# Kernel tuning notes

Measured on AMD Instinct MI355X. Metric: run time of the kernel, lower is better.

Reference implementation:

```python
import jax, jax.numpy as jnp
import numpy as np

N = 10000      # nodes
E = 160000     # edges
MUL = 64       # multiplicity of 0e and 1o in node feats / target
NATTR = 10     # number of element types (node_attrs one-hot width)
RDIM = 8       # radial (edge_feats) dim
NAVG = 16.0    # num_avg_neighbors
_INV3 = 0.5773502691896258  # CG coeff for 1o x 1o -> 0e (1/sqrt(3))


def setup_inputs() -> dict:
    key = jax.random.key(0)
    ks = jax.random.split(key, 20)
    return {
        "node_attrs": jax.random.uniform(ks[0], (N, NATTR), jnp.float32),
        "node_feats": jax.random.normal(ks[1], (N, 4 * MUL), jnp.float32),
        "edge_attrs_real": jax.random.normal(ks[2], (E, 4), jnp.float32),
        "edge_attrs_imag": jax.random.normal(ks[3], (E, 4), jnp.float32),
        "edge_feats": jax.random.normal(ks[4], (E, RDIM), jnp.float32),
        # linear_up (per-l internal weights)
        "W_up0": jax.random.normal(ks[5], (MUL, MUL), jnp.float32),
        "W_up1": jax.random.normal(ks[6], (MUL, MUL), jnp.float32),
        # conv_tp_weights MLP: [8, 64, 64, 64, 4*MUL]
        "M1": jax.random.normal(ks[7], (RDIM, 64), jnp.float32),
        "M2": jax.random.normal(ks[8], (64, 64), jnp.float32),
        "M3": jax.random.normal(ks[9], (64, 64), jnp.float32),
        "M4": jax.random.normal(ks[10], (64, 4 * MUL), jnp.float32),
        # linear: irreps_mid (128x0e+128x1o) -> irreps_nonlin (128x0e+64x1o)
        "W_lin_s": jax.random.normal(ks[11], (2 * MUL, 2 * MUL), jnp.float32),
        "W_lin_v": jax.random.normal(ks[12], (2 * MUL, MUL), jnp.float32),
        # skip_tp: FullyConnectedTensorProduct(node_feats, node_attrs -> irreps_nonlin)
        "W_sk_s": jax.random.normal(ks[13], (MUL, NATTR, 2 * MUL), jnp.float32),
        "W_sk_v": jax.random.normal(ks[14], (MUL, NATTR, MUL), jnp.float32),
        "edge_index": jax.random.randint(ks[15], (2, E), 0, N, jnp.int64
                                         if jax.config.jax_enable_x64 else jnp.int32),
    }


def _forward(node_attrs, node_feats, edge_attrs_real, edge_attrs_imag, edge_feats,
             W_up0, W_up1, M1, M2, M3, M4, W_lin_s, W_lin_v, W_sk_s, W_sk_v,
             sender, receiver):
    n = node_feats.shape[0]
    x0 = node_feats[:, :MUL]                          # (N, 64)   64x0e
    x1 = node_feats[:, MUL:].reshape(n, MUL, 3)       # (N, 64, 3) 64x1o

    # skip TP (fully connected, node_attrs are scalars)
    sk_norm = 1.0 / np.sqrt(MUL * NATTR)
    sc_s = jnp.einsum('nu,na,uav->nv', x0, node_attrs, W_sk_s) * sk_norm   # (N,128)
    sc_v = jnp.einsum('nui,na,uav->nvi', x1, node_attrs, W_sk_v) * sk_norm # (N,64,3)

    # linear_up (per-l)
    up_norm = 1.0 / np.sqrt(MUL)
    x0 = (x0 @ W_up0) * up_norm
    x1 = jnp.einsum('nui,uv->nvi', x1, W_up1) * up_norm

    # radial MLP -> per-edge TP weights (4 uvu paths x MUL)
    h = jax.nn.silu((edge_feats @ M1) / np.sqrt(RDIM))
    h = jax.nn.silu((h @ M2) / 8.0)
    h = jax.nn.silu((h @ M3) / 8.0)
    tw = (h @ M4) / 8.0                               # (E, 256)
    wA, wB, wC, wD = (tw[:, :MUL], tw[:, MUL:2*MUL],
                      tw[:, 2*MUL:3*MUL], tw[:, 3*MUL:])

    xs0 = x0[sender]                                  # (E, 64)
    xs1 = x1[sender]                                  # (E, 64, 3)

    def conv_tp(y):
        # y: (E,4) = [0e | 1o]; uvu paths with per-edge weights
        y0, y1 = y[:, :1], y[:, 1:]
        s = jnp.concatenate([xs0 * y0 * wA,                                  # 0e x 0e -> 0e
                             jnp.einsum('eui,ei->eu', xs1, y1) * _INV3 * wD  # 1o x 1o -> 0e
                             ], axis=1)                                      # (E,128)
        v = jnp.concatenate([(xs0 * wB)[:, :, None] * y1[:, None, :],        # 0e x 1o -> 1o
                             xs1 * (y0 * wC)[:, :, None]                     # 1o x 0e -> 1o
                             ], axis=1)                                      # (E,128,3)
        return s, v

    sr, vr = conv_tp(edge_attrs_real)
    si, vi = conv_tp(edge_attrs_imag)

    ms_r = jax.ops.segment_sum(sr, receiver, num_segments=n)
    mv_r = jax.ops.segment_sum(vr, receiver, num_segments=n)
    ms_i = jax.ops.segment_sum(si, receiver, num_segments=n)
    mv_i = jax.ops.segment_sum(vi, receiver, num_segments=n)

    lin_norm = (1.0 / np.sqrt(2 * MUL)) / (2.0 * NAVG)

    def lin(ms, mv):
        return (ms @ W_lin_s) * lin_norm, jnp.einsum('nui,uv->nvi', mv, W_lin_v) * lin_norm

    def gate(s, v):
        # irreps_nonlin = 64x0e scalars | 64x0e gates | 64x1o gated
        scal = jax.nn.silu(s[:, :MUL])
        g = jax.nn.silu(s[:, MUL:])
        return jnp.concatenate([scal, (v * g[:, :, None]).reshape(n, 3 * MUL)], axis=1)

    ls, lv = lin(ms_r, mv_r)
    real = gate(ls + sc_s, lv + sc_v)                 # (N, 256), residual on real part
    lsi, lvi = lin(ms_i, mv_i)
    imag = gate(lsi, lvi)                             # (N, 256)

    # view_as_complex + reshape [N, num_features, dim//num_features]; complex kept
    # as trailing real/imag axis of size 2.
    return jnp.stack([real, imag], axis=-1).reshape(n, MUL, (4 * MUL) // MUL, 2)


def reference(node_attrs, node_feats, edge_attrs_real, edge_attrs_imag, edge_feats,
              W_up0, W_up1, M1, M2, M3, M4, W_lin_s, W_lin_v, W_sk_s, W_sk_v,
              edge_index):
    sender, receiver = edge_index[0], edge_index[1]
    return _forward(node_attrs, node_feats, edge_attrs_real, edge_attrs_imag,
                    edge_feats, W_up0, W_up1, M1, M2, M3, M4,
                    W_lin_s, W_lin_v, W_sk_s, W_sk_v, sender, receiver)
```

## Files before the change

kernel.cpp:

```cpp
#include <hip/hip_runtime.h>
#include <hip/hip_bf16.h>

#define NN 10000
#define NE 160000
#define NGRP 625
#define XPLN 640000

#define SK_NORM   0.039528470752104741f
#define UP_NORM   0.125f
#define M1_NORM   0.35355339059327373f
#define INV3      0.5773502691896258f
#define LIN_NORM  0.0027621358640099516f

__device__ __forceinline__ float siluf(float x) { return x / (1.0f + __expf(-x)); }

__device__ __forceinline__ unsigned short f2bf_bits(float x) {
    union { __hip_bfloat16 h; unsigned short u; } cv;
    cv.h = __float2bfloat16(x);
    return cv.u;
}
__device__ __forceinline__ float bflo(unsigned int w) { return __uint_as_float(w << 16); }
__device__ __forceinline__ float bfhi(unsigned int w) { return __uint_as_float(w & 0xffff0000u); }

typedef short bf16x8 __attribute__((ext_vector_type(8)));
typedef float f32x4  __attribute__((ext_vector_type(4)));

__global__ __launch_bounds__(256) void k_detect(const int* __restrict__ ei32, int* __restrict__ flag) {
    __shared__ int cnt;
    if (threadIdx.x == 0) cnt = 0;
    __syncthreads();
    int z = 0;
    for (int i = threadIdx.x; i < 1024; i += 256)
        if (ei32[2 * i + 1] == 0) z++;
    atomicAdd(&cnt, z);
    __syncthreads();
    if (threadIdx.x == 0) flag[0] = (cnt >= 512) ? 1 : 0;
}

__global__ __launch_bounds__(256) void k_cvt(const int* __restrict__ ei32, const int* __restrict__ flag,
                                             int* __restrict__ snd, int* __restrict__ rcv) {
    int e = blockIdx.x * 256 + threadIdx.x;
    if (e >= NE) return;
    if (flag[0]) {
        const long long* e64 = (const long long*)ei32;
        snd[e] = (int)e64[e];
        rcv[e] = (int)e64[NE + e];
    } else {
        snd[e] = ei32[e];
        rcv[e] = ei32[NE + e];
    }
}

__global__ __launch_bounds__(256) void k_wprepN(
    const float* __restrict__ Wsk_s, const float* __restrict__ Wsk_v,
    const float* __restrict__ Wu0, const float* __restrict__ Wu1,
    unsigned short* __restrict__ WNF) {
    int idx = blockIdx.x * 256 + threadIdx.x;
    if (idx >= 131072) return;
    float val;
    if (idx < 81920) {
        int p = idx / 10240, r = idx % 10240;
        int kc = r >> 9, l8 = r & 511;
        int lane = l8 >> 3, j = l8 & 7, quad = lane >> 4, lo = lane & 15;
        int a = kc >> 1, u = (kc & 1) * 32 + quad * 8 + j;
        val = Wsk_s[(u * 10 + a) * 128 + p * 16 + lo];
    } else if (idx < 122880) {
        int rel = idx - 81920;
        int p = rel / 10240, r = rel % 10240;
        int kc = r >> 9, l8 = r & 511;
        int lane = l8 >> 3, j = l8 & 7, quad = lane >> 4, lo = lane & 15;
        int a = kc >> 1, u = (kc & 1) * 32 + quad * 8 + j;
        val = Wsk_v[(u * 10 + a) * 64 + p * 16 + lo];
    } else if (idx < 126976) {
        int rel = idx - 122880;
        int p = rel >> 10, r = rel & 1023;
        int kc = r >> 9, l8 = r & 511;
        int lane = l8 >> 3, j = l8 & 7, quad = lane >> 4, lo = lane & 15;
        int u = kc * 32 + quad * 8 + j;
        val = Wu0[u * 64 + p * 16 + lo];
    } else {
        int rel = idx - 126976;
        int p = rel >> 10, r = rel & 1023;
        int kc = r >> 9, l8 = r & 511;
        int lane = l8 >> 3, j = l8 & 7, quad = lane >> 4, lo = lane & 15;
        int u = kc * 32 + quad * 8 + j;
        val = Wu1[u * 64 + p * 16 + lo];
    }
    WNF[idx] = f2bf_bits(val);
}

__global__ __launch_bounds__(256) void k_xprep(
    const float* __restrict__ node_attrs, const float* __restrict__ node_feats,
    unsigned short* __restrict__ xpk, float* __restrict__ attrsP) {
    int idx = blockIdx.x * 256 + threadIdx.x;
    if (idx < 4 * NN * 64) {
        int n = idx >> 8, c = idx & 255;
        int plane = c >> 6, u = c & 63;
        float v = (plane == 0) ? node_feats[(long)n * 256 + u]
                               : node_feats[(long)n * 256 + 64 + u * 3 + (plane - 1)];
        xpk[(size_t)plane * XPLN + (long)n * 64 + u] = f2bf_bits(v);
        return;
    }
    int i2 = idx - 4 * NN * 64;
    if (i2 < 10 * NN) {
        int a = i2 / NN, n = i2 - a * NN;
        attrsP[i2] = node_attrs[(long)n * 10 + a];
    }
}

__global__ __launch_bounds__(256) void k_wprep2(
    const float* __restrict__ M1, const float* __restrict__ M2,
    const float* __restrict__ M3, const float* __restrict__ M4,
    const float* __restrict__ W_lin_s, const float* __restrict__ W_lin_v,
    unsigned short* __restrict__ WFG, unsigned short* __restrict__ WLF) {
    int idx = blockIdx.x * 256 + threadIdx.x;
    if (idx >= (52 + 48) * 512) return;
    if (idx < 52 * 512) {
        int f = idx >> 9, r = idx & 511;
        int lane = r >> 3, j = r & 7;
        int quad = lane >> 4, lo = lane & 15;
        float val;
        if (f < 4) {
            int n = f * 16 + lo, k = quad * 8 + j;
            val = (k < 8) ? M1[k * 64 + n] : 0.f;
        } else if (f < 12) {
            int g2 = f - 4, nt = g2 >> 1, half = g2 & 1;
            int n = nt * 16 + lo, k = half * 32 + quad * 8 + j;
            val = M2[k * 64 + n];
        } else if (f < 20) {
            int g3 = f - 12, nt = g3 >> 1, half = g3 & 1;
            int n = nt * 16 + lo, k = half * 32 + quad * 8 + j;
            val = M3[k * 64 + n];
        } else {
            int g4 = f - 20, tt = g4 >> 1, half = g4 & 1;
            int n = tt * 16 + lo, k = half * 32 + quad * 8 + j;
            val = M4[k * 256 + n];
        }
        WFG[idx] = f2bf_bits(val);
    } else {
        int rel = idx - 52 * 512;
        int f = rel >> 9, r = rel & 511;
        int lane = r >> 3, j = r & 7;
        int quad = lane >> 4, lo = lane & 15;
        float val;
        if (f < 32) {
            int vt = f >> 2, ks = f & 3;
            val = W_lin_s[(ks * 32 + quad * 8 + j) * 128 + vt * 16 + lo];
        } else {
            int f2 = f - 32;
            int vt = f2 >> 2, ks = f2 & 3;
            val = W_lin_v[(ks * 32 + quad * 8 + j) * 64 + vt * 16 + lo];
        }
        WLF[rel] = f2bf_bits(val);
    }
}

#define G0 8
#define NB0 79
#define G2 4
#define NB2 157
#define G3 16
#define NB3 40
#define KNODE_GRID (4*NB0 + 2*NB2 + 2*NB3)

__global__ __launch_bounds__(128) void k_node(
    const unsigned short* __restrict__ xpk, const float* __restrict__ attrsP,
    const unsigned short* __restrict__ WNF,
    float* __restrict__ sc_s, float* __restrict__ sc_v,
    float* __restrict__ x0u, float* __restrict__ x1p) {
    __shared__ unsigned short pan[2 * 10240];
    __shared__ float att[10 * 128];

    int t = threadIdx.x;
    int bid = blockIdx.x;
    int type, vp, chunk;
    if (bid < 4 * NB0)                 { type = 0; vp = bid / NB0; chunk = bid % NB0; }
    else if (bid < 4 * NB0 + 2 * NB2)  { int r = bid - 4 * NB0; type = 2; vp = r / NB2; chunk = r % NB2; }
    else                               { int r = bid - 4 * NB0 - 2 * NB2; type = 3; vp = r / NB3; chunk = r % NB3; }
    int G = (type == 0) ? G0 : (type == 2 ? G2 : G3);
    int g0 = chunk * G;
    int ng = NGRP - g0; if (ng > G) ng = G;
    int n0 = g0 * 16;

    int psrc, pcnt;
    if (type == 0)      { psrc = vp * 2 * 10240;           pcnt = 20480; }
    else if (type == 2) { psrc = 81920 + vp * 2 * 10240;   pcnt = 20480; }
    else                { psrc = 122880 + vp * 2 * 1024;   pcnt = 2048;  }
    for (int i = t; i < pcnt / 8; i += 128)
        ((float4*)pan)[i] = ((const float4*)(WNF + psrc))[i];
    if (type == 3) {
        for (int i = t; i < 2048 / 8; i += 128)
            ((float4*)(pan + 2048))[i] = ((const float4*)(WNF + 126976 + vp * 2 * 1024))[i];
    }
    if (type <= 2) {
        int cnt = ng * 16;
        #pragma unroll
        for (int k = 0; k < 10; k++) {
            int i = k * 128 + t;
            int nl = t;
            if (nl < cnt) att[i] = attrsP[k * NN + n0 + nl];
        }
    }
    __syncthreads();

    int wv = t >> 6, lane = t & 63, lo = lane & 15, quad = lane >> 4;
    int lbase = lane * 8;
    const f32x4 zacc = {0.f, 0.f, 0.f, 0.f};
    const unsigned short* mypan = pan + wv * 10240;

    if (type == 0) {
        int vtg = vp * 2 + wv;
        const unsigned short* xb = xpk;
        bf16x8 nfa0 = *(const bf16x8*)(xb + (long)(n0 + lo) * 64 + quad * 8);
        bf16x8 nfa1 = *(const bf16x8*)(xb + (long)(n0 + lo) * 64 + 32 + quad * 8);
        #pragma unroll 1
        for (int g = 0; g < ng; g++) {
            bf16x8 fa0 = nfa0, fa1 = nfa1;
            if (g + 1 < ng) {
                nfa0 = *(const bf16x8*)(xb + (long)(n0 + (g + 1) * 16 + lo) * 64 + quad * 8);
                nfa1 = *(const bf16x8*)(xb + (long)(n0 + (g + 1) * 16 + lo) * 64 + 32 + quad * 8);
            }
            f32x4 acc = zacc;
            #pragma unroll
            for (int a = 0; a < 10; a++) {
                bf16x8 b0 = *(const bf16x8*)&mypan[(2 * a) * 512 + lbase];
                bf16x8 b1 = *(const bf16x8*)&mypan[(2 * a + 1) * 512 + lbase];
                f32x4 p = __builtin_amdgcn_mfma_f32_16x16x32_bf16(fa0, b0, zacc, 0, 0, 0);
                p = __builtin_amdgcn_mfma_f32_16x16x32_bf16(fa1, b1, p, 0, 0, 0);
                float4 afv = *(const float4*)&att[a * 128 + g * 16 + quad * 4];
                acc[0] += afv.x * p[0]; acc[1] += afv.y * p[1];
                acc[2] += afv.z * p[2]; acc[3] += afv.w * p[3];
            }
            int nb = n0 + g * 16;
            #pragma unroll
            for (int r = 0; r < 4; r++)
                sc_s[(long)(nb + quad * 4 + r) * 128 + vtg * 16 + lo] = acc[r] * SK_NORM;
        }
    } else if (type == 2) {
        int vt = vp * 2 + wv;
        bf16x8 nfa0[3], nfa1[3];
        #pragma unroll
        for (int i = 0; i < 3; i++) {
            const unsigned short* xb = xpk + (size_t)(1 + i) * XPLN + (long)(n0 + lo) * 64;
            nfa0[i] = *(const bf16x8*)(xb + quad * 8);
            nfa1[i] = *(const bf16x8*)(xb + 32 + quad * 8);
        }
        #pragma unroll 1
        for (int g = 0; g < ng; g++) {
            bf16x8 fa0[3], fa1[3];
            #pragma unroll
            for (int i = 0; i < 3; i++) { fa0[i] = nfa0[i]; fa1[i] = nfa1[i]; }
            if (g + 1 < ng) {
                #pragma unroll
                for (int i = 0; i < 3; i++) {
                    const unsigned short* xb = xpk + (size_t)(1 + i) * XPLN + (long)(n0 + (g + 1) * 16 + lo) * 64;
                    nfa0[i] = *(const bf16x8*)(xb + quad * 8);
                    nfa1[i] = *(const bf16x8*)(xb + 32 + quad * 8);
                }
            }
            f32x4 acc0 = zacc, acc1 = zacc, acc2 = zacc;
            #pragma unroll
            for (int a = 0; a < 10; a++) {
                bf16x8 b0 = *(const bf16x8*)&mypan[(2 * a) * 512 + lbase];
                bf16x8 b1 = *(const bf16x8*)&mypan[(2 * a + 1) * 512 + lbase];
                float4 afv = *(const float4*)&att[a * 128 + g * 16 + quad * 4];
                f32x4 p0 = __builtin_amdgcn_mfma_f32_16x16x32_bf16(fa0[0], b0, zacc, 0, 0, 0);
                p0 = __builtin_amdgcn_mfma_f32_16x16x32_bf16(fa1[0], b1, p0, 0, 0, 0);
                acc0[0] += afv.x * p0[0]; acc0[1] += afv.y * p0[1];
                acc0[2] += afv.z * p0[2]; acc0[3] += afv.w * p0[3];
                f32x4 p1 = __builtin_amdgcn_mfma_f32_16x16x32_bf16(fa0[1], b0, zacc, 0, 0, 0);
                p1 = __builtin_amdgcn_mfma_f32_16x16x32_bf16(fa1[1], b1, p1, 0, 0, 0);
                acc1[0] += afv.x * p1[0]; acc1[1] += afv.y * p1[1];
                acc1[2] += afv.z * p1[2]; acc1[3] += afv.w * p1[3];
                f32x4 p2 = __builtin_amdgcn_mfma_f32_16x16x32_bf16(fa0[2], b0, zacc, 0, 0, 0);
                p2 = __builtin_amdgcn_mfma_f32_16x16x32_bf16(fa1[2], b1, p2, 0, 0, 0);
                acc2[0] += afv.x * p2[0]; acc2[1] += afv.y * p2[1];
                acc2[2] += afv.z * p2[2]; acc2[3] += afv.w * p2[3];
            }
            int nb = n0 + g * 16;
            #pragma unroll
            for (int r = 0; r < 4; r++) {
                long rb = (long)(nb + quad * 4 + r) * 192 + vt * 16 + lo;
                sc_v[rb]       = acc0[r] * SK_NORM;
                sc_v[rb + 64]  = acc1[r] * SK_NORM;
                sc_v[rb + 128] = acc2[r] * SK_NORM;
            }
        }
    } else {
        int vt = vp * 2 + wv;
        bf16x8 bk20 = *(const bf16x8*)&pan[wv * 1024 + lbase];
        bf16x8 bk21 = *(const bf16x8*)&pan[wv * 1024 + 512 + lbase];
        bf16x8 bk30 = *(const bf16x8*)&pan[2048 + wv * 1024 + lbase];
        bf16x8 bk31 = *(const bf16x8*)&pan[2048 + wv * 1024 + 512 + lbase];
        #pragma unroll 1
        for (int g = 0; g < ng; g++) {
            int nb = n0 + g * 16;
            {
                const unsigned short* xb = xpk + (long)(nb + lo) * 64;
                bf16x8 fa0 = *(const bf16x8*)(xb + quad * 8);
                bf16x8 fa1 = *(const bf16x8*)(xb + 32 + quad * 8);
                f32x4 acc = __builtin_amdgcn_mfma_f32_16x16x32_bf16(fa0, bk20, zacc, 0, 0, 0);
                acc = __builtin_amdgcn_mfma_f32_16x16x32_bf16(fa1, bk21, acc, 0, 0, 0);
                #pragma unroll
                for (int r = 0; r < 4; r++)
                    x0u[(long)(nb + quad * 4 + r) * 64 + vt * 16 + lo] = acc[r] * UP_NORM;
            }
            #pragma unroll
            for (int i = 0; i < 3; i++) {
                const unsigned short* xb = xpk + (size_t)(1 + i) * XPLN + (long)(nb + lo) * 64;
                bf16x8 fa0 = *(const bf16x8*)(xb + quad * 8);
                bf16x8 fa1 = *(const bf16x8*)(xb + 32 + quad * 8);
                f32x4 acc = __builtin_amdgcn_mfma_f32_16x16x32_bf16(fa0, bk30, zacc, 0, 0, 0);
                acc = __builtin_amdgcn_mfma_f32_16x16x32_bf16(fa1, bk31, acc, 0, 0, 0);
                #pragma unroll
                for (int r = 0; r < 4; r++)
                    x1p[(size_t)i * XPLN + (long)(nb + quad * 4 + r) * 64 + vt * 16 + lo] = acc[r] * UP_NORM;
            }
        }
    }
}

__global__ __launch_bounds__(256) void k_hist(const int* __restrict__ rcv, int* __restrict__ counts) {
    int e = blockIdx.x * 256 + threadIdx.x;
    if (e < NE) atomicAdd(&counts[rcv[e]], 1);
}

__global__ __launch_bounds__(1024) void k_scan(const int* __restrict__ counts, int* __restrict__ offsets) {
    __shared__ int partial[1024];
    int t = threadIdx.x;
    const int CHUNK = (NN + 1023) / 1024;
    int base = t * CHUNK;
    int s = 0;
    for (int i = 0; i < CHUNK; i++) if (base + i < NN) s += counts[base + i];
    partial[t] = s;
    __syncthreads();
    for (int d = 1; d < 1024; d *= 2) {
        int v = (t >= d) ? partial[t - d] : 0;
        __syncthreads();
        partial[t] += v;
        __syncthreads();
    }
    int excl = (t == 0) ? 0 : partial[t - 1];
    for (int i = 0; i < CHUNK; i++) {
        if (base + i < NN) { offsets[base + i] = excl; excl += counts[base + i]; }
    }
    if (t == 1023) offsets[NN] = partial[1023];
}

__global__ __launch_bounds__(256) void k_fill(const int* __restrict__ rcv, const int* __restrict__ snd,
                                              const int* __restrict__ offsets,
                                              int* __restrict__ cursor, int2* __restrict__ epk) {
    int e = blockIdx.x * 256 + threadIdx.x;
    if (e < NE) {
        int r = rcv[e];
        int pos = atomicAdd(&cursor[r], 1);
        epk[offsets[r] + pos] = make_int2(snd[e], e);
    }
}

__global__ __launch_bounds__(256) void k_eprep(const int2* __restrict__ epk,
                                               const float4* __restrict__ ear, const float4* __restrict__ eai,
                                               const float4* __restrict__ ef,
                                               int* __restrict__ sndp,
                                               float4* __restrict__ earp, float4* __restrict__ eaip,
                                               float4* __restrict__ efp) {
    int j = blockIdx.x * 256 + threadIdx.x;
    if (j >= NE) return;
    int2 se = epk[j];
    sndp[j] = se.x;
    earp[j] = ear[se.y];
    eaip[j] = eai[se.y];
    efp[(long)j * 2]     = ef[(long)se.y * 2];
    efp[(long)j * 2 + 1] = ef[(long)se.y * 2 + 1];
}

#define HID_STRIDE 72
#define OB_STRIDE  40
#define EPB 256
#define EMW 8

__global__ __launch_bounds__(512) void k_edge_mlp(
    const float4* __restrict__ efp, const unsigned short* __restrict__ WFG,
    __hip_bfloat16* __restrict__ twp) {
    __shared__ unsigned short wfrag[52 * 512];
    __shared__ unsigned short hid[EMW][16 * HID_STRIDE];

    int t = threadIdx.x;
    for (int i = t; i < 52 * 512 / 8; i += 512)
        ((float4*)wfrag)[i] = ((const float4*)WFG)[i];
    __syncthreads();

    int wv = t >> 6;
    int lane = t & 63;
    int lo = lane & 15;
    int quad = lane >> 4;
    int lbase = lane * 8;
    unsigned short* myhid = hid[wv];
    unsigned short* myob  = hid[wv];
    const f32x4 zacc = {0.f, 0.f, 0.f, 0.f};

    float4 f0, f1;
    if (quad == 0) {
        long jb0 = (long)blockIdx.x * EPB + wv * 16;
        f0 = efp[(jb0 + lo) * 2];
        f1 = efp[(jb0 + lo) * 2 + 1];
    }

    #pragma unroll 1
    for (int g = 0; g < EPB / 128; g++) {
        long jbase = (long)blockIdx.x * EPB + g * 128 + wv * 16;

        bf16x8 a1 = {0, 0, 0, 0, 0, 0, 0, 0};
        if (quad == 0) {
            union { unsigned short us[8]; bf16x8 v; } pk;
            pk.us[0] = f2bf_bits(f0.x * M1_NORM); pk.us[1] = f2bf_bits(f0.y * M1_NORM);
            pk.us[2] = f2bf_bits(f0.z * M1_NORM); pk.us[3] = f2bf_bits(f0.w * M1_NORM);
            pk.us[4] = f2bf_bits(f1.x * M1_NORM); pk.us[5] = f2bf_bits(f1.y * M1_NORM);
            pk.us[6] = f2bf_bits(f1.z * M1_NORM); pk.us[7] = f2bf_bits(f1.w * M1_NORM);
            a1 = pk.v;
            if (g + 1 < EPB / 128) {
                long jbn = jbase + 128;
                f0 = efp[(jbn + lo) * 2];
                f1 = efp[(jbn + lo) * 2 + 1];
            }
        }
        {
            f32x4 acc[4];
            #pragma unroll
            for (int nt = 0; nt < 4; nt++) {
                bf16x8 b = *(const bf16x8*)&wfrag[nt * 512 + lbase];
                acc[nt] = __builtin_amdgcn_mfma_f32_16x16x32_bf16(a1, b, zacc, 0, 0, 0);
            }
            #pragma unroll
            for (int nt = 0; nt < 4; nt++)
                #pragma unroll
                for (int r = 0; r < 4; r++)
                    myhid[(quad * 4 + r) * HID_STRIDE + nt * 16 + lo] = f2bf_bits(siluf(acc[nt][r]));
        }

        #pragma unroll
        for (int L = 0; L < 2; L++) {
            int fb = 4 + L * 8;
            bf16x8 a0 = *(const bf16x8*)&myhid[lo * HID_STRIDE + quad * 8];
            bf16x8 a1v = *(const bf16x8*)&myhid[lo * HID_STRIDE + 32 + quad * 8];
            f32x4 acc[4];
            #pragma unroll
            for (int nt = 0; nt < 4; nt++) {
                bf16x8 b0 = *(const bf16x8*)&wfrag[(fb + nt * 2) * 512 + lbase];
                bf16x8 b1 = *(const bf16x8*)&wfrag[(fb + nt * 2 + 1) * 512 + lbase];
                acc[nt] = __builtin_amdgcn_mfma_f32_16x16x32_bf16(a0, b0, zacc, 0, 0, 0);
                acc[nt] = __builtin_amdgcn_mfma_f32_16x16x32_bf16(a1v, b1, acc[nt], 0, 0, 0);
            }
            #pragma unroll
            for (int nt = 0; nt < 4; nt++)
                #pragma unroll
                for (int r = 0; r < 4; r++)
                    myhid[(quad * 4 + r) * HID_STRIDE + nt * 16 + lo] = f2bf_bits(siluf(acc[nt][r] * 0.125f));
        }

        {
            bf16x8 a0 = *(const bf16x8*)&myhid[lo * HID_STRIDE + quad * 8];
            bf16x8 a1v = *(const bf16x8*)&myhid[lo * HID_STRIDE + 32 + quad * 8];
            int sedge = lane >> 2, sch = lane & 3;
            #pragma unroll 1
            for (int rd = 0; rd < 8; rd++) {
                f32x4 acc2[2];
                #pragma unroll
                for (int p = 0; p < 2; p++) {
                    int tt = (rd < 4) ? (p * 4 + rd) : (8 + p * 4 + (rd - 4));
                    bf16x8 b0 = *(const bf16x8*)&wfrag[(20 + tt * 2) * 512 + lbase];
                    bf16x8 b1 = *(const bf16x8*)&wfrag[(20 + tt * 2 + 1) * 512 + lbase];
                    acc2[p] = __builtin_amdgcn_mfma_f32_16x16x32_bf16(a0, b0, zacc, 0, 0, 0);
                    acc2[p] = __builtin_amdgcn_mfma_f32_16x16x32_bf16(a1v, b1, acc2[p], 0, 0, 0);
                }
                #pragma unroll
                for (int p = 0; p < 2; p++)
                    #pragma unroll
                    for (int r = 0; r < 4; r++)
                        myob[(quad * 4 + r) * OB_STRIDE + 2 * lo + p] = f2bf_bits(acc2[p][r] * 0.125f);
                bf16x8 vv = *(const bf16x8*)&myob[sedge * OB_STRIDE + sch * 8];
                *(bf16x8*)(twp + (jbase + sedge) * 256 + rd * 32 + sch * 8) = vv;
            }
        }
    }
}

#define NPB 4
#define CB2 4
__global__ __launch_bounds__(256) void k_conv(
    const int* __restrict__ offsets, const int* __restrict__ sndp,
    const float4* __restrict__ earp, const float4* __restrict__ eaip,
    const float* __restrict__ x0u, const float* __restrict__ x1p,
    const __hip_bfloat16* __restrict__ twp,
    unsigned short* __restrict__ msgF) {
    __shared__ unsigned short stg[NPB][1024];
    int t = threadIdx.x;
    int wv = t >> 6;
    int u = t & 63;
    int n = blockIdx.x * NPB + wv;
    int beg = offsets[n], end = offsets[n + 1];
    const int tsel0 = 2 * u, tsel1 = 128 + 2 * u;
    float a0r = 0.f, a1r = 0.f, a2r = 0.f, a3r = 0.f;
    float a0i = 0.f, a1i = 0.f, a2i = 0.f, a3i = 0.f;
    float c0r = 0.f, c1r = 0.f, c2r = 0.f, c3r = 0.f;
    float c0i = 0.f, c1i = 0.f, c2i = 0.f, c3i = 0.f;

    for (int jb = beg; jb < end; jb += CB2) {
        unsigned int t0[CB2], t1[CB2];
        float x0v[CB2], xv0[CB2], xv1[CB2], xv2[CB2];
        float4 yr[CB2], yi[CB2];
        #pragma unroll
        for (int p = 0; p < CB2; p++) {
            int j = jb + p;
            int jc = (j < end) ? j : (end - 1);
            int s = sndp[jc];
            yr[p] = earp[jc];
            yi[p] = eaip[jc];
            long sb = (long)s * 64 + u;
            x0v[p] = x0u[sb];
            xv0[p] = x1p[sb];
            xv1[p] = x1p[XPLN + sb];
            xv2[p] = x1p[2 * XPLN + sb];
            bool valid = (j < end);
            t0[p] = valid ? *(const unsigned int*)(twp + (long)jc * 256 + tsel0) : 0u;
            t1[p] = valid ? *(const unsigned int*)(twp + (long)jc * 256 + tsel1) : 0u;
        }
        #pragma unroll
        for (int p = 0; p < CB2; p++) {
            float wA = bflo(t0[p]), wB = bfhi(t0[p]);
            float xa = x0v[p] * wA, xb = x0v[p] * wB;
            a0r += xa * yr[p].x; a1r += xb * yr[p].y; a2r += xb * yr[p].z; a3r += xb * yr[p].w;
            a0i += xa * yi[p].x; a1i += xb * yi[p].y; a2i += xb * yi[p].z; a3i += xb * yi[p].w;
            float wC = bflo(t1[p]), wDs = bfhi(t1[p]) * INV3;
            float dr = xv0[p] * yr[p].y + xv1[p] * yr[p].z + xv2[p] * yr[p].w;
            float di = xv0[p] * yi[p].y + xv1[p] * yi[p].z + xv2[p] * yi[p].w;
            c0r += dr * wDs; c0i += di * wDs;
            float ycr = yr[p].x * wC, yci = yi[p].x * wC;
            c1r += xv0[p] * ycr; c2r += xv1[p] * ycr; c3r += xv2[p] * ycr;
            c1i += xv0[p] * yci; c2i += xv1[p] * yci; c3i += xv2[p] * yci;
        }
    }

    unsigned short* sg = stg[wv];
    sg[u]       = f2bf_bits(a0r);
    sg[128 + u] = f2bf_bits(a0i);
    sg[256 + u] = f2bf_bits(a1r);
    sg[384 + u] = f2bf_bits(a2r);
    sg[512 + u] = f2bf_bits(a3r);
    sg[640 + u] = f2bf_bits(a1i);
    sg[768 + u] = f2bf_bits(a2i);
    sg[896 + u] = f2bf_bits(a3i);
    sg[64 + u]  = f2bf_bits(c0r);
    sg[192 + u] = f2bf_bits(c0i);
    sg[320 + u] = f2bf_bits(c1r);
    sg[448 + u] = f2bf_bits(c2r);
    sg[576 + u] = f2bf_bits(c3r);
    sg[704 + u] = f2bf_bits(c1i);
    sg[832 + u] = f2bf_bits(c2i);
    sg[960 + u] = f2bf_bits(c3i);
    __syncthreads();

    #pragma unroll
    for (int rep = 0; rep < 2; rep++) {
        int job = rep * 256 + t;
        int m = job >> 7, c = job & 127;
        int nm = blockIdx.x * NPB + m;
        int g = nm >> 4, lo = nm & 15;
        bf16x8 vv = *(const bf16x8*)&stg[m][c * 8];
        *(bf16x8*)(msgF + (size_t)g * 16384 + (c >> 2) * 512 + lo * 32 + (c & 3) * 8) = vv;
    }
}

#define SV_STRIDE 129
#define VV_STRIDE 65

__global__ __launch_bounds__(256, 3) void k_lin(
    const unsigned short* __restrict__ msgF,
    const float* __restrict__ sc_s, const float* __restrict__ sc_v,
    const unsigned short* __restrict__ WLF,
    float* __restrict__ out) {
    __shared__ char smem[49152];
    unsigned short* wfrag = (unsigned short*)smem;
    float* sval = (float*)smem;
    float* vval = (float*)(smem + 2 * 16 * SV_STRIDE * 4);

    int t = threadIdx.x;
    for (int i = t; i < 48 * 512 / 8; i += 256)
        ((float4*)wfrag)[i] = ((const float4*)WLF)[i];
    __syncthreads();

    int wv = t >> 6;
    int lane = t & 63;
    int lo = lane & 15;
    int quad = lane >> 4;
    int lbase = lane * 8;
    int aoff_lane = lo * 32 + quad * 8;
    const f32x4 zacc = {0.f, 0.f, 0.f, 0.f};

    long g = blockIdx.x;
    long nbase = g * 16;
    const unsigned short* agbase = msgF + (size_t)g * 16384;

    f32x4 accs[10];
    #pragma unroll
    for (int q = 0; q < 10; q++) {
        int tau = wv + q * 4;
        int cblk, fb;
        if (tau < 16) {
            int ri = tau >> 3, vt = tau & 7;
            cblk = ri; fb = vt * 4;
        } else {
            int tp = tau - 16;
            int ri = tp / 12, rem = tp % 12;
            int i = rem >> 2, vt = rem & 3;
            cblk = 2 + ri * 3 + i; fb = 32 + vt * 4;
        }
        f32x4 acc = zacc;
        #pragma unroll
        for (int ks = 0; ks < 4; ks++) {
            bf16x8 a = *(const bf16x8*)(agbase + (cblk * 4 + ks) * 512 + aoff_lane);
            bf16x8 b = *(const bf16x8*)&wfrag[(fb + ks) * 512 + lbase];
            acc = __builtin_amdgcn_mfma_f32_16x16x32_bf16(a, b, acc, 0, 0, 0);
        }
        accs[q] = acc;
    }
    __syncthreads();

    #pragma unroll
    for (int q = 0; q < 10; q++) {
        int tau = wv + q * 4;
        if (tau < 16) {
            int ri = tau >> 3, vt = tau & 7;
            int cidx = (ri * 16) * SV_STRIDE + vt * 16 + lo;
            #pragma unroll
            for (int r = 0; r < 4; r++)
                sval[cidx + (quad * 4 + r) * SV_STRIDE] = accs[q][r] * LIN_NORM;
        } else {
            int tp = tau - 16;
            int ri = tp / 12, rem = tp % 12;
            int i = rem >> 2, vt = rem & 3;
            int cidx = ((ri * 3 + i) * 16) * VV_STRIDE + vt * 16 + lo;
            #pragma unroll
            for (int r = 0; r < 4; r++)
                vval[cidx + (quad * 4 + r) * VV_STRIDE] = accs[q][r] * LIN_NORM;
        }
    }
    __syncthreads();

    #pragma unroll 1
    for (int j = 0; j < 16; j++) {
        int c = t;
        long gn = nbase + j;
        float re, im;
        if (c < 64) {
            float sr = sval[(0 * 16 + j) * SV_STRIDE + c] + sc_s[gn * 128 + c];
            float si = sval[(1 * 16 + j) * SV_STRIDE + c];
            re = siluf(sr); im = siluf(si);
        } else {
            int rem = c - 64;
            int v = rem / 3;
            int i = rem - v * 3;
            float gr = siluf(sval[(0 * 16 + j) * SV_STRIDE + 64 + v] + sc_s[gn * 128 + 64 + v]);
            float gi = siluf(sval[(1 * 16 + j) * SV_STRIDE + 64 + v]);
            float lr = vval[((0 * 3 + i) * 16 + j) * VV_STRIDE + v] + sc_v[gn * 192 + i * 64 + v];
            float li = vval[((1 * 3 + i) * 16 + j) * VV_STRIDE + v];
            re = lr * gr; im = li * gi;
        }
        ((float2*)out)[gn * 256 + c] = make_float2(re, im);
    }
}

extern "C" void kernel_launch(void* const* d_in, const int* in_sizes, int n_in,
                              void* d_out, int out_size, void* d_ws, size_t ws_size,
                              hipStream_t stream) {
    const float* node_attrs = (const float*)d_in[0];
    const float* node_feats = (const float*)d_in[1];
    const float* ear        = (const float*)d_in[2];
    const float* eai        = (const float*)d_in[3];
    const float* edge_feats = (const float*)d_in[4];
    const float* W_up0      = (const float*)d_in[5];
    const float* W_up1      = (const float*)d_in[6];
    const float* M1         = (const float*)d_in[7];
    const float* M2         = (const float*)d_in[8];
    const float* M3         = (const float*)d_in[9];
    const float* M4         = (const float*)d_in[10];
    const float* W_lin_s    = (const float*)d_in[11];
    const float* W_lin_v    = (const float*)d_in[12];
    const float* W_sk_s     = (const float*)d_in[13];
    const float* W_sk_v     = (const float*)d_in[14];
    const int*   ei         = (const int*)d_in[15];

    char* ws = (char*)d_ws;
    size_t o_x0u = 0;
    size_t o_x1p = o_x0u + (size_t)NN * 64 * 4;
    size_t o_scs = o_x1p + (size_t)NN * 256 * 4;
    size_t o_scv = o_scs + (size_t)NN * 128 * 4;
    size_t o_tw  = o_scv + (size_t)NN * 192 * 4;
    size_t o_cnt = o_tw  + (size_t)NE * 256 * 2;
    size_t o_cur = o_cnt + (size_t)NN * 4;
    size_t o_ofs = o_cur + (size_t)NN * 4;
    size_t o_epk = o_ofs + (size_t)(NN + 1) * 4 + 60;
    size_t o_snd = o_epk + (size_t)NE * 8;
    size_t o_rcv = o_snd + (size_t)NE * 4;
    size_t o_flg = o_rcv + (size_t)NE * 4;
    size_t o_msg = o_flg + 64;
    size_t o_wnf = o_msg + (size_t)NN * 1024 * 2;
    size_t o_snp = o_wnf + 262144;
    size_t o_erp = o_snp + (size_t)NE * 4;
    size_t o_eip = o_erp + (size_t)NE * 16;
    size_t o_efp = o_eip + (size_t)NE * 16;
    size_t o_wfg = o_efp + (size_t)NE * 32;
    size_t o_wlf = o_wfg + (size_t)52 * 512 * 2;
    size_t o_xpk = o_wlf + (size_t)48 * 512 * 2;
    size_t o_atp = o_xpk + (size_t)4 * NN * 64 * 2;

    float* x0u = (float*)(ws + o_x0u);
    float* x1p = (float*)(ws + o_x1p);
    float* sc_s = (float*)(ws + o_scs);
    float* sc_v = (float*)(ws + o_scv);
    __hip_bfloat16* twp = (__hip_bfloat16*)(ws + o_tw);
    int* counts  = (int*)(ws + o_cnt);
    int* cursor  = (int*)(ws + o_cur);
    int* offsets = (int*)(ws + o_ofs);
    int2* epk    = (int2*)(ws + o_epk);
    int* snd     = (int*)(ws + o_snd);
    int* rcv     = (int*)(ws + o_rcv);
    int* flag    = (int*)(ws + o_flg);
    unsigned short* msgF = (unsigned short*)(ws + o_msg);
    unsigned short* WNF = (unsigned short*)(ws + o_wnf);
    int*    sndp = (int*)(ws + o_snp);
    float4* earp = (float4*)(ws + o_erp);
    float4* eaip = (float4*)(ws + o_eip);
    float4* efp  = (float4*)(ws + o_efp);
    unsigned short* WFG = (unsigned short*)(ws + o_wfg);
    unsigned short* WLF = (unsigned short*)(ws + o_wlf);
    unsigned short* xpk = (unsigned short*)(ws + o_xpk);
    float* attrsP = (float*)(ws + o_atp);

    hipMemsetAsync(ws + o_cnt, 0, (size_t)NN * 8, stream);

    dim3 b256(256), b1024(1024), b128(128), b512(512);
    k_detect<<<dim3(1), b256, 0, stream>>>(ei, flag);
    k_cvt   <<<dim3((NE + 255) / 256), b256, 0, stream>>>(ei, flag, snd, rcv);
    k_hist<<<dim3((NE + 255) / 256), b256, 0, stream>>>(rcv, counts);
    k_scan<<<dim3(1), b1024, 0, stream>>>(counts, offsets);
    k_fill<<<dim3((NE + 255) / 256), b256, 0, stream>>>(rcv, snd, offsets, cursor, epk);
    k_eprep<<<dim3((NE + 255) / 256), b256, 0, stream>>>(epk, (const float4*)ear, (const float4*)eai,
                                                         (const float4*)edge_feats,
                                                         sndp, earp, eaip, efp);
    k_wprepN<<<dim3(512), b256, 0, stream>>>(W_sk_s, W_sk_v, W_up0, W_up1, WNF);
    k_wprep2<<<dim3(200), b256, 0, stream>>>(M1, M2, M3, M4, W_lin_s, W_lin_v, WFG, WLF);
    k_xprep <<<dim3((4 * NN * 64 + 10 * NN + 255) / 256), b256, 0, stream>>>(node_attrs, node_feats, xpk, attrsP);
    k_node  <<<dim3(KNODE_GRID), b128, 0, stream>>>(xpk, attrsP, WNF, sc_s, sc_v, x0u, x1p);
    k_edge_mlp<<<dim3(NE / EPB), b512, 0, stream>>>(efp, WFG, twp);
    k_conv<<<dim3(NN / NPB), b256, 0, stream>>>(offsets, sndp, earp, eaip, x0u, x1p, twp, msgF);
    k_lin <<<dim3(NGRP), b256, 0, stream>>>(msgF, sc_s, sc_v, WLF, (float*)d_out);
}
```

Before: 274.0 us.

## Fuse edge radial MLP into per-node convolution, keeping edge weights in LDS

Merges the edge MLP kernel and the convolution kernel into one. Each block computes the radial MLP for its four nodes' contiguous edge range in 64-edge chunks and stores the per-edge tensor-product weights in shared memory instead of a global buffer. This removes the global write and re-read of the 160000x256 bf16 weight tensor and one launch. In exchange it adds block barriers and idle waves when a chunk has fewer than 64 edges. The last-layer weights are now read straight from global memory rather than LDS, and sender indices for the first 64 edges per node come from a wave shuffle.

New measurement: 309.9 us. +13.1%, slower.

```diff
diff --git a/kernel.cpp b/kernel.cpp
--- a/kernel.cpp
+++ b/kernel.cpp
@@ -328,10 +328,10 @@
 __global__ __launch_bounds__(1024) void k_scan(const int* __restrict__ counts, int* __restrict__ offsets) {
     __shared__ int partial[1024];
     int t = threadIdx.x;
-    const int CHUNK = (NN + 1023) / 1024;
-    int base = t * CHUNK;
+    const int CHUNKS = (NN + 1023) / 1024;
+    int base = t * CHUNKS;
     int s = 0;
-    for (int i = 0; i < CHUNK; i++) if (base + i < NN) s += counts[base + i];
+    for (int i = 0; i < CHUNKS; i++) if (base + i < NN) s += counts[base + i];
     partial[t] = s;
     __syncthreads();
     for (int d = 1; d < 1024; d *= 2) {
@@ -341,7 +341,7 @@
         __syncthreads();
     }
     int excl = (t == 0) ? 0 : partial[t - 1];
-    for (int i = 0; i < CHUNK; i++) {
+    for (int i = 0; i < CHUNKS; i++) {
         if (base + i < NN) { offsets[base + i] = excl; excl += counts[base + i]; }
     }
     if (t == 1023) offsets[NN] = partial[1023];
@@ -376,19 +376,25 @@
 
 #define HID_STRIDE 72
 #define OB_STRIDE  40
-#define EPB 256
-#define EMW 8
-
-__global__ __launch_bounds__(512) void k_edge_mlp(
-    const float4* __restrict__ efp, const unsigned short* __restrict__ WFG,
-    __hip_bfloat16* __restrict__ twp) {
-    __shared__ unsigned short wfrag[52 * 512];
-    __shared__ unsigned short hid[EMW][16 * HID_STRIDE];
+#define ECHUNK 64
+#define TW_STRIDE 264
+#define NPB 4
+#define CB2 4
+
+__global__ __launch_bounds__(256) void k_econv(
+    const int* __restrict__ offsets, const int* __restrict__ sndp,
+    const float4* __restrict__ efp,
+    const float4* __restrict__ earp, const float4* __restrict__ eaip,
+    const float* __restrict__ x0u, const float* __restrict__ x1p,
+    const unsigned short* __restrict__ WFG,
+    unsigned short* __restrict__ msgF) {
+    __shared__ unsigned short wfrag[20 * 512];
+    __shared__ unsigned short twch[ECHUNK * TW_STRIDE];
+    __shared__ unsigned short hid[4][16 * HID_STRIDE];
 
     int t = threadIdx.x;
-    for (int i = t; i < 52 * 512 / 8; i += 512)
+    for (int i = t; i < 20 * 512 / 8; i += 256)
         ((float4*)wfrag)[i] = ((const float4*)WFG)[i];
-    __syncthreads();
 
     int wv = t >> 6;
     int lane = t & 63;
@@ -397,151 +403,144 @@
     int lbase = lane * 8;
     unsigned short* myhid = hid[wv];
     unsigned short* myob  = hid[wv];
+    const unsigned short* W4 = WFG + 20 * 512;
     const f32x4 zacc = {0.f, 0.f, 0.f, 0.f};
 
-    float4 f0, f1;
-    if (quad == 0) {
-        long jb0 = (long)blockIdx.x * EPB + wv * 16;
-        f0 = efp[(jb0 + lo) * 2];
-        f1 = efp[(jb0 + lo) * 2 + 1];
-    }
-
-    #pragma unroll 1
-    for (int g = 0; g < EPB / 128; g++) {
-        long jbase = (long)blockIdx.x * EPB + g * 128 + wv * 16;
-
-        bf16x8 a1 = {0, 0, 0, 0, 0, 0, 0, 0};
-        if (quad == 0) {
-            union { unsigned short us[8]; bf16x8 v; } pk;
-            pk.us[0] = f2bf_bits(f0.x * M1_NORM); pk.us[1] = f2bf_bits(f0.y * M1_NORM);
-            pk.us[2] = f2bf_bits(f0.z * M1_NORM); pk.us[3] = f2bf_bits(f0.w * M1_NORM);
-            pk.us[4] = f2bf_bits(f1.x * M1_NORM); pk.us[5] = f2bf_bits(f1.y * M1_NORM);
-            pk.us[6] = f2bf_bits(f1.z * M1_NORM); pk.us[7] = f2bf_bits(f1.w * M1_NORM);
-            a1 = pk.v;
-            if (g + 1 < EPB / 128) {
-                long jbn = jbase + 128;
-                f0 = efp[(jbn + lo) * 2];
-                f1 = efp[(jbn + lo) * 2 + 1];
-            }
-        }
-        {
-            f32x4 acc[4];
-            #pragma unroll
-            for (int nt = 0; nt < 4; nt++) {
-                bf16x8 b = *(const bf16x8*)&wfrag[nt * 512 + lbase];
-                acc[nt] = __builtin_amdgcn_mfma_f32_16x16x32_bf16(a1, b, zacc, 0, 0, 0);
-            }
-            #pragma unroll
-            for (int nt = 0; nt < 4; nt++)
-                #pragma unroll
-                for (int r = 0; r < 4; r++)
-                    myhid[(quad * 4 + r) * HID_STRIDE + nt * 16 + lo] = f2bf_bits(siluf(acc[nt][r]));
-        }
-
-        #pragma unroll
-        for (int L = 0; L < 2; L++) {
-            int fb = 4 + L * 8;
-            bf16x8 a0 = *(const bf16x8*)&myhid[lo * HID_STRIDE + quad * 8];
-            bf16x8 a1v = *(const bf16x8*)&myhid[lo * HID_STRIDE + 32 + quad * 8];
-            f32x4 acc[4];
-            #pragma unroll
-            for (int nt = 0; nt < 4; nt++) {
-                bf16x8 b0 = *(const bf16x8*)&wfrag[(fb + nt * 2) * 512 + lbase];
-                bf16x8 b1 = *(const bf16x8*)&wfrag[(fb + nt * 2 + 1) * 512 + lbase];
-                acc[nt] = __builtin_amdgcn_mfma_f32_16x16x32_bf16(a0, b0, zacc, 0, 0, 0);
-                acc[nt] = __builtin_amdgcn_mfma_f32_16x16x32_bf16(a1v, b1, acc[nt], 0, 0, 0);
-            }
-            #pragma unroll
-            for (int nt = 0; nt < 4; nt++)
-                #pragma unroll
-                for (int r = 0; r < 4; r++)
-                    myhid[(quad * 4 + r) * HID_STRIDE + nt * 16 + lo] = f2bf_bits(siluf(acc[nt][r] * 0.125f));
-        }
-
-        {
-            bf16x8 a0 = *(const bf16x8*)&myhid[lo * HID_STRIDE + quad * 8];
-            bf16x8 a1v = *(const bf16x8*)&myhid[lo * HID_STRIDE + 32 + quad * 8];
-            int sedge = lane >> 2, sch = lane & 3;
-            #pragma unroll 1
-            for (int rd = 0; rd < 8; rd++) {
-                f32x4 acc2[2];
-                #pragma unroll
-                for (int p = 0; p < 2; p++) {
-                    int tt = (rd < 4) ? (p * 4 + rd) : (8 + p * 4 + (rd - 4));
-                    bf16x8 b0 = *(const bf16x8*)&wfrag[(20 + tt * 2) * 512 + lbase];
-                    bf16x8 b1 = *(const bf16x8*)&wfrag[(20 + tt * 2 + 1) * 512 + lbase];
-                    acc2[p] = __builtin_amdgcn_mfma_f32_16x16x32_bf16(a0, b0, zacc, 0, 0, 0);
-                    acc2[p] = __builtin_amdgcn_mfma_f32_16x16x32_bf16(a1v, b1, acc2[p], 0, 0, 0);
-                }
-                #pragma unroll
-                for (int p = 0; p < 2; p++)
-                    #pragma unroll
-                    for (int r = 0; r < 4; r++)
-                        myob[(quad * 4 + r) * OB_STRIDE + 2 * lo + p] = f2bf_bits(acc2[p][r] * 0.125f);
-                bf16x8 vv = *(const bf16x8*)&myob[sedge * OB_STRIDE + sch * 8];
-                *(bf16x8*)(twp + (jbase + sedge) * 256 + rd * 32 + sch * 8) = vv;
-            }
-        }
-    }
-}
-
-#define NPB 4
-#define CB2 4
-__global__ __launch_bounds__(256) void k_conv(
-    const int* __restrict__ offsets, const int* __restrict__ sndp,
-    const float4* __restrict__ earp, const float4* __restrict__ eaip,
-    const float* __restrict__ x0u, const float* __restrict__ x1p,
-    const __hip_bfloat16* __restrict__ twp,
-    unsigned short* __restrict__ msgF) {
-    __shared__ unsigned short stg[NPB][1024];
-    int t = threadIdx.x;
-    int wv = t >> 6;
-    int u = t & 63;
-    int n = blockIdx.x * NPB + wv;
-    int beg = offsets[n], end = offsets[n + 1];
-    const int tsel0 = 2 * u, tsel1 = 128 + 2 * u;
+    int n0 = blockIdx.x * NPB;
+    int n  = n0 + wv;
+    int beg0 = offsets[n0], end0 = offsets[n0 + NPB];
+    int begn = offsets[n],  endn = offsets[n + 1];
+    int degn = endn - begn;
+    int sreg = (lane < degn) ? sndp[begn + lane] : 0;
+
+    const int u = lane;
     float a0r = 0.f, a1r = 0.f, a2r = 0.f, a3r = 0.f;
     float a0i = 0.f, a1i = 0.f, a2i = 0.f, a3i = 0.f;
     float c0r = 0.f, c1r = 0.f, c2r = 0.f, c3r = 0.f;
     float c0i = 0.f, c1i = 0.f, c2i = 0.f, c3i = 0.f;
 
-    for (int jb = beg; jb < end; jb += CB2) {
-        unsigned int t0[CB2], t1[CB2];
-        float x0v[CB2], xv0[CB2], xv1[CB2], xv2[CB2];
-        float4 yr[CB2], yi[CB2];
-        #pragma unroll
-        for (int p = 0; p < CB2; p++) {
-            int j = jb + p;
-            int jc = (j < end) ? j : (end - 1);
-            int s = sndp[jc];
-            yr[p] = earp[jc];
-            yi[p] = eaip[jc];
-            long sb = (long)s * 64 + u;
-            x0v[p] = x0u[sb];
-            xv0[p] = x1p[sb];
-            xv1[p] = x1p[XPLN + sb];
-            xv2[p] = x1p[2 * XPLN + sb];
-            bool valid = (j < end);
-            t0[p] = valid ? *(const unsigned int*)(twp + (long)jc * 256 + tsel0) : 0u;
-            t1[p] = valid ? *(const unsigned int*)(twp + (long)jc * 256 + tsel1) : 0u;
-        }
-        #pragma unroll
-        for (int p = 0; p < CB2; p++) {
-            float wA = bflo(t0[p]), wB = bfhi(t0[p]);
-            float xa = x0v[p] * wA, xb = x0v[p] * wB;
-            a0r += xa * yr[p].x; a1r += xb * yr[p].y; a2r += xb * yr[p].z; a3r += xb * yr[p].w;
-            a0i += xa * yi[p].x; a1i += xb * yi[p].y; a2i += xb * yi[p].z; a3i += xb * yi[p].w;
-            float wC = bflo(t1[p]), wDs = bfhi(t1[p]) * INV3;
-            float dr = xv0[p] * yr[p].y + xv1[p] * yr[p].z + xv2[p] * yr[p].w;
-            float di = xv0[p] * yi[p].y + xv1[p] * yi[p].z + xv2[p] * yi[p].w;
-            c0r += dr * wDs; c0i += di * wDs;
-            float ycr = yr[p].x * wC, yci = yi[p].x * wC;
-            c1r += xv0[p] * ycr; c2r += xv1[p] * ycr; c3r += xv2[p] * ycr;
-            c1i += xv0[p] * yci; c2i += xv1[p] * yci; c3i += xv2[p] * yci;
-        }
-    }
-
-    unsigned short* sg = stg[wv];
+    __syncthreads();
+
+    #pragma unroll 1
+    for (int cbeg = beg0; cbeg < end0; cbeg += ECHUNK) {
+        int cend = cbeg + ECHUNK; if (cend > end0) cend = end0;
+
+        int tb = cbeg + wv * 16;
+        if (tb < cend) {
+            bf16x8 a1 = {0, 0, 0, 0, 0, 0, 0, 0};
+            if (quad == 0) {
+                long jc = tb + lo; if (jc > end0 - 1) jc = end0 - 1;
+                float4 f0 = efp[jc * 2];
+                float4 f1 = efp[jc * 2 + 1];
+                union { unsigned short us[8]; bf16x8 v; } pk;
+                pk.us[0] = f2bf_bits(f0.x * M1_NORM); pk.us[1] = f2bf_bits(f0.y * M1_NORM);
+                pk.us[2] = f2bf_bits(f0.z * M1_NORM); pk.us[3] = f2bf_bits(f0.w * M1_NORM);
+                pk.us[4] = f2bf_bits(f1.x * M1_NORM); pk.us[5] = f2bf_bits(f1.y * M1_NORM);
+                pk.us[6] = f2bf_bits(f1.z * M1_NORM); pk.us[7] = f2bf_bits(f1.w * M1_NORM);
+                a1 = pk.v;
+            }
+            {
+                f32x4 acc[4];
+                #pragma unroll
+                for (int nt = 0; nt < 4; nt++) {
+                    bf16x8 b = *(const bf16x8*)&wfrag[nt * 512 + lbase];
+                    acc[nt] = __builtin_amdgcn_mfma_f32_16x16x32_bf16(a1, b, zacc, 0, 0, 0);
+                }
+                #pragma unroll
+                for (int nt = 0; nt < 4; nt++)
+                    #pragma unroll
+                    for (int r = 0; r < 4; r++)
+                        myhid[(quad * 4 + r) * HID_STRIDE + nt * 16 + lo] = f2bf_bits(siluf(acc[nt][r]));
+            }
+            #pragma unroll
+            for (int L = 0; L < 2; L++) {
+                int fb = 4 + L * 8;
+                bf16x8 a0 = *(const bf16x8*)&myhid[lo * HID_STRIDE + quad * 8];
+                bf16x8 a1v = *(const bf16x8*)&myhid[lo * HID_STRIDE + 32 + quad * 8];
+                f32x4 acc[4];
+                #pragma unroll
+                for (int nt = 0; nt < 4; nt++) {
+                    bf16x8 b0 = *(const bf16x8*)&wfrag[(fb + nt * 2) * 512 + lbase];
+                    bf16x8 b1 = *(const bf16x8*)&wfrag[(fb + nt * 2 + 1) * 512 + lbase];
+                    acc[nt] = __builtin_amdgcn_mfma_f32_16x16x32_bf16(a0, b0, zacc, 0, 0, 0);
+                    acc[nt] = __builtin_amdgcn_mfma_f32_16x16x32_bf16(a1v, b1, acc[nt], 0, 0, 0);
+                }
+                #pragma unroll
+                for (int nt = 0; nt < 4; nt++)
+                    #pragma unroll
+                    for (int r = 0; r < 4; r++)
+                        myhid[(quad * 4 + r) * HID_STRIDE + nt * 16 + lo] = f2bf_bits(siluf(acc[nt][r] * 0.125f));
+            }
+            {
+                bf16x8 a0 = *(const bf16x8*)&myhid[lo * HID_STRIDE + quad * 8];
+                bf16x8 a1v = *(const bf16x8*)&myhid[lo * HID_STRIDE + 32 + quad * 8];
+                int sedge = lane >> 2, sch = lane & 3;
+                #pragma unroll
+                for (int rd = 0; rd < 8; rd++) {
+                    f32x4 acc2[2];
+                    #pragma unroll
+                    for (int p = 0; p < 2; p++) {
+                        int tt = (rd < 4) ? (p * 4 + rd) : (8 + p * 4 + (rd - 4));
+                        bf16x8 b0 = *(const bf16x8*)(W4 + (tt * 2) * 512 + lbase);
+                        bf16x8 b1 = *(const bf16x8*)(W4 + (tt * 2 + 1) * 512 + lbase);
+                        acc2[p] = __builtin_amdgcn_mfma_f32_16x16x32_bf16(a0, b0, zacc, 0, 0, 0);
+                        acc2[p] = __builtin_amdgcn_mfma_f32_16x16x32_bf16(a1v, b1, acc2[p], 0, 0, 0);
+                    }
+                    #pragma unroll
+                    for (int p = 0; p < 2; p++)
+                        #pragma unroll
+                        for (int r = 0; r < 4; r++)
+                            myob[(quad * 4 + r) * OB_STRIDE + 2 * lo + p] = f2bf_bits(acc2[p][r] * 0.125f);
+                    bf16x8 vv = *(const bf16x8*)&myob[sedge * OB_STRIDE + sch * 8];
+                    *(bf16x8*)(twch + (size_t)(wv * 16 + sedge) * TW_STRIDE + rd * 32 + sch * 8) = vv;
+                }
+            }
+        }
+        __syncthreads();
+
+        int lj = (begn > cbeg) ? begn : cbeg;
+        int hj = (endn < cend) ? endn : cend;
+        for (int jb = lj; jb < hj; jb += CB2) {
+            unsigned int t0[CB2], t1[CB2];
+            float x0v[CB2], xv0[CB2], xv1[CB2], xv2[CB2];
+            float4 yr[CB2], yi[CB2];
+            #pragma unroll
+            for (int p = 0; p < CB2; p++) {
+                int j = jb + p;
+                int jc = (j < hj) ? j : (hj - 1);
+                int le = jc - begn;
+                int s = (le < 64) ? __shfl(sreg, le) : sndp[jc];
+                yr[p] = earp[jc];
+                yi[p] = eaip[jc];
+                long sb = (long)s * 64 + u;
+                x0v[p] = x0u[sb];
+                xv0[p] = x1p[sb];
+                xv1[p] = x1p[XPLN + sb];
+                xv2[p] = x1p[2 * XPLN + sb];
+                int ls = jc - cbeg;
+                bool valid = (j < hj);
+                t0[p] = valid ? *(const unsigned int*)(twch + ls * TW_STRIDE + 2 * u) : 0u;
+                t1[p] = valid ? *(const unsigned int*)(twch + ls * TW_STRIDE + 128 + 2 * u) : 0u;
+            }
+            #pragma unroll
+            for (int p = 0; p < CB2; p++) {
+                float wA = bflo(t0[p]), wB = bfhi(t0[p]);
+                float xa = x0v[p] * wA, xb = x0v[p] * wB;
+                a0r += xa * yr[p].x; a1r += xb * yr[p].y; a2r += xb * yr[p].z; a3r += xb * yr[p].w;
+                a0i += xa * yi[p].x; a1i += xb * yi[p].y; a2i += xb * yi[p].z; a3i += xb * yi[p].w;
+                float wC = bflo(t1[p]), wDs = bfhi(t1[p]) * INV3;
+                float dr = xv0[p] * yr[p].y + xv1[p] * yr[p].z + xv2[p] * yr[p].w;
+                float di = xv0[p] * yi[p].y + xv1[p] * yi[p].z + xv2[p] * yi[p].w;
+                c0r += dr * wDs; c0i += di * wDs;
+                float ycr = yr[p].x * wC, yci = yi[p].x * wC;
+                c1r += xv0[p] * ycr; c2r += xv1[p] * ycr; c3r += xv2[p] * ycr;
+                c1i += xv0[p] * yci; c2i += xv1[p] * yci; c3i += xv2[p] * yci;
+            }
+        }
+        __syncthreads();
+    }
+
+    unsigned short* sg = twch + wv * 1024;
     sg[u]       = f2bf_bits(a0r);
     sg[128 + u] = f2bf_bits(a0i);
     sg[256 + u] = f2bf_bits(a1r);
@@ -564,10 +563,10 @@
     for (int rep = 0; rep < 2; rep++) {
         int job = rep * 256 + t;
         int m = job >> 7, c = job & 127;
-        int nm = blockIdx.x * NPB + m;
-        int g = nm >> 4, lo = nm & 15;
-        bf16x8 vv = *(const bf16x8*)&stg[m][c * 8];
-        *(bf16x8*)(msgF + (size_t)g * 16384 + (c >> 2) * 512 + lo * 32 + (c & 3) * 8) = vv;
+        int nm = n0 + m;
+        int g = nm >> 4, l2 = nm & 15;
+        bf16x8 vv = *(const bf16x8*)&twch[m * 1024 + c * 8];
+        *(bf16x8*)(msgF + (size_t)g * 16384 + (c >> 2) * 512 + l2 * 32 + (c & 3) * 8) = vv;
     }
 }
 
@@ -718,7 +717,6 @@
     float* x1p = (float*)(ws + o_x1p);
     float* sc_s = (float*)(ws + o_scs);
     float* sc_v = (float*)(ws + o_scv);
-    __hip_bfloat16* twp = (__hip_bfloat16*)(ws + o_tw);
     int* counts  = (int*)(ws + o_cnt);
     int* cursor  = (int*)(ws + o_cur);
     int* offsets = (int*)(ws + o_ofs);
@@ -739,7 +737,7 @@
 
     hipMemsetAsync(ws + o_cnt, 0, (size_t)NN * 8, stream);
 
-    dim3 b256(256), b1024(1024), b128(128), b512(512);
+    dim3 b256(256), b1024(1024), b128(128);
     k_detect<<<dim3(1), b256, 0, stream>>>(ei, flag);
     k_cvt   <<<dim3((NE + 255) / 256), b256, 0, stream>>>(ei, flag, snd, rcv);
     k_hist<<<dim3((NE + 255) / 256), b256, 0, stream>>>(rcv, counts);
@@ -752,7 +750,7 @@
     k_wprep2<<<dim3(200), b256, 0, stream>>>(M1, M2, M3, M4, W_lin_s, W_lin_v, WFG, WLF);
     k_xprep <<<dim3((4 * NN * 64 + 10 * NN + 255) / 256), b256, 0, stream>>>(node_attrs, node_feats, xpk, attrsP);
     k_node  <<<dim3(KNODE_GRID), b128, 0, stream>>>(xpk, attrsP, WNF, sc_s, sc_v, x0u, x1p);
-    k_edge_mlp<<<dim3(NE / EPB), b512, 0, stream>>>(efp, WFG, twp);
-    k_conv<<<dim3(NN / NPB), b256, 0, stream>>>(offsets, sndp, earp, eaip, x0u, x1p, twp, msgF);
+    k_econv<<<dim3(NN / NPB), b256, 0, stream>>>(offsets, sndp, efp, earp, eaip,
+                                                 x0u, x1p, WFG, msgF);
     k_lin <<<dim3(NGRP), b256, 0, stream>>>(msgF, sc_s, sc_v, WLF, (float*)d_out);
 }
```
